# Kernel optimization log

Hardware: AMD Instinct MI355X
Metric: run time of the kernel (lower is better)

## Reference

```python
import jax, jax.numpy as jnp
import numpy as np
import math

DIM = 1024
NUM_HEADS = 16
HEAD_DIM = DIM // NUM_HEADS  # 64
LAYER_IDX = 12
LAMBDA_INIT = 0.8 - 0.6 * math.exp(-0.3 * (LAYER_IDX - 1))
LN_EPS = 1e-5


def setup_inputs() -> dict:
    key = jax.random.key(0)
    ks = jax.random.split(key, 11)
    B, S = 2, 2048
    x = jax.random.normal(ks[0], (B, S, DIM), dtype=jnp.float32)
    s = 1.0 / math.sqrt(DIM)
    Wq = jax.random.normal(ks[1], (DIM, 2 * DIM), dtype=jnp.float32) * s
    Wk = jax.random.normal(ks[2], (DIM, 2 * DIM), dtype=jnp.float32) * s
    Wv = jax.random.normal(ks[3], (DIM, DIM), dtype=jnp.float32) * s
    Wo = jax.random.normal(ks[4], (DIM, DIM), dtype=jnp.float32) * s
    lambda_q1 = jax.random.normal(ks[5], (HEAD_DIM,), dtype=jnp.float32) * 0.1
    lambda_k1 = jax.random.normal(ks[6], (HEAD_DIM,), dtype=jnp.float32) * 0.1
    lambda_q2 = jax.random.normal(ks[7], (HEAD_DIM,), dtype=jnp.float32) * 0.1
    lambda_k2 = jax.random.normal(ks[8], (HEAD_DIM,), dtype=jnp.float32) * 0.1
    gamma = jnp.ones((DIM,), dtype=jnp.float32)
    beta = jnp.zeros((DIM,), dtype=jnp.float32)
    return {"x": x, "Wq": Wq, "Wk": Wk, "Wv": Wv, "Wo": Wo,
            "lambda_q1": lambda_q1, "lambda_k1": lambda_k1,
            "lambda_q2": lambda_q2, "lambda_k2": lambda_k2,
            "gamma": gamma, "beta": beta}


def reference(x, Wq, Wk, Wv, Wo, lambda_q1, lambda_k1, lambda_q2, lambda_k2, gamma, beta):
    B, S, _ = x.shape
    scaling = HEAD_DIM ** (-0.5)
    # projections: [B,S,H,2d] / [B,S,H,d] -> [B,H,S,*]
    Q = (x @ Wq).reshape(B, S, NUM_HEADS, 2 * HEAD_DIM).transpose(0, 2, 1, 3)
    K = (x @ Wk).reshape(B, S, NUM_HEADS, 2 * HEAD_DIM).transpose(0, 2, 1, 3)
    V = (x @ Wv).reshape(B, S, NUM_HEADS, HEAD_DIM).transpose(0, 2, 1, 3)
    # lambda scalar
    lamb = (jnp.exp(jnp.sum(lambda_q1 * lambda_k1))
            - jnp.exp(jnp.sum(lambda_q2 * lambda_k2)) + LAMBDA_INIT)
    Q1, Q2 = jnp.split(Q, 2, axis=-1)
    K1, K2 = jnp.split(K, 2, axis=-1)
    A1 = jnp.einsum('bhqd,bhkd->bhqk', Q1, K1) * scaling
    A2 = jnp.einsum('bhqd,bhkd->bhqk', Q2, K2) * scaling
    attn = jax.nn.softmax(A1, axis=-1) - lamb * jax.nn.softmax(A2, axis=-1)
    out = jnp.einsum('bhqk,bhkd->bhqd', attn, V)  # [B,H,S,d]
    out = out.transpose(0, 2, 1, 3).reshape(B, S, DIM)
    out = out @ Wo
    # LayerNorm
    mu = jnp.mean(out, axis=-1, keepdims=True)
    var = jnp.var(out, axis=-1, keepdims=True)
    out = (out - mu) * jax.lax.rsqrt(var + LN_EPS) * gamma + beta
    return out
```

## Files before the change

### kernel.cpp

```cpp
#include <hip/hip_runtime.h>
#include <hip/hip_bf16.h>

typedef short bf16x8 __attribute__((ext_vector_type(8)));
typedef float f32x4 __attribute__((ext_vector_type(4)));
typedef unsigned short us4v __attribute__((ext_vector_type(4)));
typedef unsigned int uint2v __attribute__((ext_vector_type(2)));

#define DEV static __device__ __forceinline__

DEV float bf2f(unsigned short u){ unsigned int x = ((unsigned int)u)<<16; float f; __builtin_memcpy(&f,&x,4); return f; }
DEV unsigned short f2bf(float f){ unsigned int x; __builtin_memcpy(&x,&f,4); x = (x + 0x7fffu + ((x>>16)&1u)) >> 16; return (unsigned short)x; }

#if __has_builtin(__builtin_amdgcn_perm)
DEV unsigned int pack_trunc(float lo, float hi){
  unsigned int a, b;
  __builtin_memcpy(&a, &lo, 4);
  __builtin_memcpy(&b, &hi, 4);
  return __builtin_amdgcn_perm(b, a, 0x07060302u);
}
#else
DEV unsigned int pack_trunc(float lo, float hi){
  unsigned int a, b;
  __builtin_memcpy(&a, &lo, 4);
  __builtin_memcpy(&b, &hi, 4);
  return (b & 0xffff0000u) | (a >> 16);
}
#endif

DEV void stor(unsigned short* p, float v){ *p = f2bf(v); }
DEV void stor(float* p, float v){ *p = v; }

#if __has_builtin(__builtin_amdgcn_exp2f)
DEV float fexp2(float x){ return __builtin_amdgcn_exp2f(x); }
#else
DEV float fexp2(float x){ return exp2f(x); }
#endif

#if __has_builtin(__builtin_amdgcn_permlane32_swap)
DEV uint2v pl32(unsigned int a, unsigned int b){ return __builtin_amdgcn_permlane32_swap(a, b, false, false); }
#else
DEV uint2v pl32(unsigned int a, unsigned int b){
  unsigned int sa = (unsigned int)__shfl_xor((int)a, 32);
  unsigned int sb = (unsigned int)__shfl_xor((int)b, 32);
  bool hi = (threadIdx.x & 32) != 0;
  uint2v r; r[0] = hi ? sb : a; r[1] = hi ? b : sa; return r;
}
#endif
#if __has_builtin(__builtin_amdgcn_permlane16_swap)
DEV uint2v pl16(unsigned int a, unsigned int b){ return __builtin_amdgcn_permlane16_swap(a, b, false, false); }
#else
DEV uint2v pl16(unsigned int a, unsigned int b){
  unsigned int sa = (unsigned int)__shfl_xor((int)a, 16);
  unsigned int sb = (unsigned int)__shfl_xor((int)b, 16);
  bool hi = (threadIdx.x & 16) != 0;
  uint2v r; r[0] = hi ? sb : a; r[1] = hi ? b : sa; return r;
}
#endif

#define GLOAD_LDS16(gptr, lptr) \
  __builtin_amdgcn_global_load_lds((__attribute__((address_space(1))) void*)(gptr), \
      (__attribute__((address_space(3))) void*)(lptr), 16, 0, 0)

template<typename OutT>
__global__ __launch_bounds__(256) void gemm_bt(
    const unsigned short* __restrict__ A,
    const unsigned short* __restrict__ Bt,
    OutT* __restrict__ C, int M, int N, int K)
{
  __shared__ unsigned short As[128*32];
  __shared__ unsigned short Bs[128*32];
  const int tid = threadIdx.x;
  const int w = tid>>6, l = tid&63, g = l>>4, q = l&15;
  const int m0 = blockIdx.x*128, n0 = blockIdx.y*128;
  f32x4 acc[4][4];
  const f32x4 fz = {0.f,0.f,0.f,0.f};
  for (int i=0;i<4;i++) for(int j=0;j<4;j++) acc[i][j] = fz;
  for (int k0 = 0; k0 < K; k0 += 32) {
    __syncthreads();
    #pragma unroll
    for (int r = 0; r < 2; ++r) {
      int p = r*4096 + tid*16;
      int row = p>>6, colb = p&63;
      const char* ga = (const char*)(A  + (size_t)(m0+row)*K + k0) + colb;
      const char* gb = (const char*)(Bt + (size_t)(n0+row)*K + k0) + colb;
      GLOAD_LDS16(ga, (char*)As + r*4096 + w*1024);
      GLOAD_LDS16(gb, (char*)Bs + r*4096 + w*1024);
    }
    __syncthreads();
    bf16x8 af[4], bfr[4];
    #pragma unroll
    for (int i=0;i<4;i++){
      af[i]  = *(const bf16x8*)&As[((w>>1)*64 + i*16 + q)*32 + g*8];
      bfr[i] = *(const bf16x8*)&Bs[((w&1)*64 + i*16 + q)*32 + g*8];
    }
    #pragma unroll
    for (int i=0;i<4;i++)
      #pragma unroll
      for (int j=0;j<4;j++)
        acc[i][j] = __builtin_amdgcn_mfma_f32_16x16x32_bf16(af[i], bfr[j], acc[i][j], 0,0,0);
  }
  #pragma unroll
  for (int i=0;i<4;i++)
    #pragma unroll
    for (int j=0;j<4;j++)
      #pragma unroll
      for (int v=0;v<4;v++){
        int row = m0 + (w>>1)*64 + i*16 + g*4 + v;
        int col = n0 + (w&1)*64 + j*16 + q;
        stor(&C[(size_t)row*N + col], acc[i][j][v]);
      }
}

__global__ __launch_bounds__(256) void gemm_bt_64(
    const unsigned short* __restrict__ A,
    const unsigned short* __restrict__ Bt,
    float* __restrict__ C, int M, int N, int K)
{
  __shared__ unsigned short As[64*32];
  __shared__ unsigned short Bs[128*32];
  const int tid = threadIdx.x;
  const int w = tid>>6, l = tid&63, g = l>>4, q = l&15;
  const int m0 = blockIdx.x*64, n0 = blockIdx.y*128;
  f32x4 acc[4][2];
  const f32x4 fz = {0.f,0.f,0.f,0.f};
  for (int i=0;i<4;i++) for(int j=0;j<2;j++) acc[i][j] = fz;
  for (int k0 = 0; k0 < K; k0 += 32) {
    __syncthreads();
    {
      int row = tid>>2, colb = (tid&3)*16;
      const char* ga = (const char*)(A + (size_t)(m0+row)*K + k0) + colb;
      GLOAD_LDS16(ga, (char*)As + tid*16);
    }
    #pragma unroll
    for (int r = 0; r < 2; ++r) {
      int p = r*4096 + tid*16;
      int row = p>>6, colb = p&63;
      const char* gb = (const char*)(Bt + (size_t)(n0+row)*K + k0) + colb;
      GLOAD_LDS16(gb, (char*)Bs + r*4096 + w*1024);
    }
    __syncthreads();
    bf16x8 af[4], bfr[2];
    #pragma unroll
    for (int i=0;i<4;i++) af[i] = *(const bf16x8*)&As[(i*16 + q)*32 + g*8];
    #pragma unroll
    for (int j=0;j<2;j++) bfr[j] = *(const bf16x8*)&Bs[(w*32 + j*16 + q)*32 + g*8];
    #pragma unroll
    for (int i=0;i<4;i++)
      #pragma unroll
      for (int j=0;j<2;j++)
        acc[i][j] = __builtin_amdgcn_mfma_f32_16x16x32_bf16(af[i], bfr[j], acc[i][j], 0,0,0);
  }
  #pragma unroll
  for (int i=0;i<4;i++)
    #pragma unroll
    for (int j=0;j<2;j++)
      #pragma unroll
      for (int v=0;v<4;v++){
        int row = m0 + i*16 + g*4 + v;
        int col = n0 + w*32 + j*16 + q;
        C[(size_t)row*N + col] = acc[i][j][v];
      }
}

__global__ __launch_bounds__(256,4) void diff_attn(
    const unsigned short* __restrict__ Qp,
    const unsigned short* __restrict__ Kp,
    const unsigned short* __restrict__ Vt,
    unsigned short* __restrict__ ao1,
    unsigned short* __restrict__ ao2)
{
  const int LDQ = 5120;
  __shared__ unsigned short Ks0[64*64];
  __shared__ unsigned short Ks1[64*64];
  __shared__ unsigned short Vs0[64*64];
  __shared__ unsigned short Vs1[64*64];
  const int tid = threadIdx.x, w = tid>>6, l = tid&63, g = l>>4, q = l&15;
  const int qb = blockIdx.x, h = blockIdx.y;
  const int s = blockIdx.z >> 1, b = blockIdx.z & 1;
  const int b2048 = b*2048;
  const int qrow0 = b2048 + qb*128 + w*32;
  const f32x4 fz = {0.f,0.f,0.f,0.f};
  const short one_bf = (short)0x3f80;
  const bf16x8 ones = {one_bf,one_bf,one_bf,one_bf,one_bf,one_bf,one_bf,one_bf};
  unsigned short* aout = s ? ao2 : ao1;

  bf16x8 qf[2][2];
  #pragma unroll
  for (int qh=0; qh<2; ++qh){
    const unsigned short* qp = Qp + (size_t)(qrow0 + qh*16 + q)*LDQ + h*128 + s*64;
    #pragma unroll
    for (int kf=0;kf<2;kf++)
      qf[qh][kf] = *(const bf16x8*)(qp + kf*32 + g*8);
  }
  f32x4 acc[2][4];
  f32x4 acc_s[2];
  #pragma unroll
  for (int qh=0;qh<2;qh++){
    acc_s[qh]=fz;
    #pragma unroll
    for (int i=0;i<4;i++) acc[qh][i]=fz;
  }

  auto STAGE = [&](unsigned short* Kd, unsigned short* Vd, int kt){
    #pragma unroll
    for (int ii=0; ii<2; ++ii){
      int krow = w*16 + ii*8 + (l>>3);
      int gr = (l&7) ^ (krow&7);
      const unsigned short* src = Kp + (size_t)(b2048 + kt + krow)*LDQ + h*128 + s*64 + gr*8;
      GLOAD_LDS16(src, (char*)Kd + (w*16 + ii*8)*128);
    }
    #pragma unroll
    for (int jj=0; jj<2; ++jj){
      int vrow = w*16 + jj*8 + (l>>3);
      int gr = (l&7) ^ (vrow&7);
      const unsigned short* src = Vt + (size_t)(h*64 + vrow)*4096 + b2048 + kt + gr*8;
      GLOAD_LDS16(src, (char*)Vd + (w*16 + jj*8)*128);
    }
  };

  auto COMPUTE = [&](const unsigned short* Kr, const unsigned short* Vr){
    const int sw = q & 7;
    unsigned int cc[2][4][2];
    #pragma unroll
    for (int fn=0; fn<4; ++fn) {
      const unsigned short* kr = Kr + (fn*16 + q)*64;
      bf16x8 kb0 = *(const bf16x8*)&kr[((0+g)^sw)*8];
      bf16x8 kb1 = *(const bf16x8*)&kr[((4+g)^sw)*8];
      f32x4 z[2];
      __builtin_amdgcn_s_setprio(1);
      #pragma unroll
      for (int qh=0; qh<2; ++qh){
        f32x4 a = fz;
        a = __builtin_amdgcn_mfma_f32_16x16x32_bf16(kb0, qf[qh][0], a, 0,0,0);
        a = __builtin_amdgcn_mfma_f32_16x16x32_bf16(kb1, qf[qh][1], a, 0,0,0);
        z[qh] = a;
      }
      __builtin_amdgcn_s_setprio(0);
      #pragma unroll
      for (int qh=0; qh<2; ++qh){
        cc[qh][fn][0] = pack_trunc(fexp2(z[qh][0]), fexp2(z[qh][1]));
        cc[qh][fn][1] = pack_trunc(fexp2(z[qh][2]), fexp2(z[qh][3]));
      }
    }

    bf16x8 pa[2][2];
    #pragma unroll
    for (int qh=0; qh<2; ++qh)
      #pragma unroll
      for (int kh=0; kh<2; ++kh){
        unsigned int* u = (unsigned int*)&pa[qh][kh];
        #pragma unroll
        for (int j=0;j<2;j++){
          uint2v d = pl32(cc[qh][2*kh][j], cc[qh][2*kh+1][j]);
          uint2v e = pl16(d[0], d[1]);
          u[j] = e[0]; u[2+j] = e[1];
        }
      }

    __builtin_amdgcn_s_setprio(1);
    #pragma unroll
    for (int kh=0; kh<2; ++kh){
      #pragma unroll
      for (int qh=0; qh<2; ++qh)
        acc_s[qh] = __builtin_amdgcn_mfma_f32_16x16x32_bf16(pa[qh][kh], ones, acc_s[qh], 0,0,0);
      #pragma unroll
      for (int fd=0; fd<4; ++fd){
        bf16x8 vb = *(const bf16x8*)&Vr[(fd*16+q)*64 + ((kh*4+g)^sw)*8];
        #pragma unroll
        for (int qh=0; qh<2; ++qh)
          acc[qh][fd] = __builtin_amdgcn_mfma_f32_16x16x32_bf16(pa[qh][kh], vb, acc[qh][fd], 0,0,0);
      }
    }
    __builtin_amdgcn_s_setprio(0);
  };

  STAGE(Ks0, Vs0, 0);
  __syncthreads();

  for (int t=0; t<32; t+=2) {
    STAGE(Ks1, Vs1, (t+1)*64);
    COMPUTE(Ks0, Vs0);
    __syncthreads();
    if (t+2 < 32) STAGE(Ks0, Vs0, (t+2)*64);
    COMPUTE(Ks1, Vs1);
    if (t+2 < 32) __syncthreads();
  }

  #pragma unroll
  for (int qh=0; qh<2; ++qh){
    float inv[4];
    #pragma unroll
    for (int i=0;i<4;i++) inv[i] = 1.0f/acc_s[qh][i];
    #pragma unroll
    for (int fd=0; fd<4; ++fd)
      #pragma unroll
      for (int i=0;i<4;i++){
        int row = qrow0 + qh*16 + g*4 + i;
        int col = h*64 + fd*16 + q;
        aout[(size_t)row*1024 + col] = f2bf(acc[qh][fd][i]*inv[i]);
      }
  }
}

__global__ __launch_bounds__(256) void combine_k(
    const unsigned short* __restrict__ a1, const unsigned short* __restrict__ a2,
    const float* __restrict__ lambp, unsigned short* __restrict__ out, int n)
{
  int i = (blockIdx.x*256 + threadIdx.x)*8;
  if (i >= n) return;
  float lamb = lambp[0];
  bf16x8 v1 = *(const bf16x8*)(a1+i), v2 = *(const bf16x8*)(a2+i);
  bf16x8 o;
  #pragma unroll
  for (int e=0;e<8;e++)
    o[e] = (short)f2bf(bf2f((unsigned short)v1[e]) - lamb*bf2f((unsigned short)v2[e]));
  *(bf16x8*)(out+i) = o;
}

__global__ __launch_bounds__(256) void f32_to_bf16_k(const float* __restrict__ in, unsigned short* __restrict__ out, int n){
  int i = (blockIdx.x*256 + threadIdx.x)*4;
  if (i >= n) return;
  float4 vv = *(const float4*)(in + i);
  us4v o; o[0]=f2bf(vv.x); o[1]=f2bf(vv.y); o[2]=f2bf(vv.z); o[3]=f2bf(vv.w);
  *(us4v*)(out + i) = o;
}

__global__ void transpose_weights(const float* __restrict__ Wq, const float* __restrict__ Wk,
                                  const float* __restrict__ Wv, const float* __restrict__ Wo,
                                  unsigned short* __restrict__ WcatT, unsigned short* __restrict__ WoT,
                                  float qscale){
  __shared__ unsigned short t[32][33];
  int bid = blockIdx.x;
  const float* in; unsigned short* out; int C; float scale = 1.0f;
  if (bid < 2048){ in = Wq; out = WcatT;             C = 2048; scale = qscale; }
  else if (bid < 4096){ in = Wk; out = WcatT + 2048*1024; C = 2048; bid -= 2048; }
  else if (bid < 5120){ in = Wv; out = WcatT + 4096*1024; C = 1024; bid -= 4096; }
  else { in = Wo; out = WoT; C = 1024; bid -= 5120; }
  int xt = (C == 2048) ? (bid & 63) : (bid & 31);
  int yt = (C == 2048) ? (bid >> 6) : (bid >> 5);
  int c0 = xt*32, r0 = yt*32;
  int x = threadIdx.x, y = threadIdx.y;
  #pragma unroll
  for (int d=0; d<32; d+=8) t[y+d][x] = f2bf(in[(size_t)(r0+y+d)*C + c0 + x] * scale);
  __syncthreads();
  #pragma unroll
  for (int d=0; d<32; d+=8) out[(size_t)(c0+y+d)*1024 + r0 + x] = t[x][y+d];
}

__global__ void transpose_bf16_ld(const unsigned short* __restrict__ in, unsigned short* __restrict__ out, int R, int C, int ldin){
  __shared__ unsigned short t[32][33];
  int c0 = blockIdx.x*32, r0 = blockIdx.y*32;
  int x = threadIdx.x, y = threadIdx.y;
  #pragma unroll
  for (int d=0; d<32; d+=8) t[y+d][x] = in[(size_t)(r0+y+d)*ldin + c0 + x];
  __syncthreads();
  #pragma unroll
  for (int d=0; d<32; d+=8) out[(size_t)(c0+y+d)*R + r0 + x] = t[x][y+d];
}

__global__ void lamb_k(const float* lq1, const float* lk1, const float* lq2, const float* lk2, float* out){
  int i = threadIdx.x;
  float a = lq1[i]*lk1[i], c = lq2[i]*lk2[i];
  #pragma unroll
  for (int o=32;o>0;o>>=1){ a += __shfl_down(a,o); c += __shfl_down(c,o); }
  if (i==0) out[0] = expf(a) - expf(c) + 0.7778700995592560f;
}

__global__ __launch_bounds__(256) void ln_k(const float* __restrict__ in, const float* __restrict__ gam,
                                            const float* __restrict__ bet, float* __restrict__ out){
  int row = blockIdx.x, t = threadIdx.x;
  const float4* rp = (const float4*)(in + (size_t)row*1024);
  float4 v4 = rp[t];
  float s = v4.x+v4.y+v4.z+v4.w;
  float ss = v4.x*v4.x+v4.y*v4.y+v4.z*v4.z+v4.w*v4.w;
  #pragma unroll
  for (int o=1;o<64;o<<=1){ s += __shfl_xor(s,o); ss += __shfl_xor(ss,o); }
  __shared__ float red[8];
  int w = t>>6, l = t&63;
  if (l==0){ red[w]=s; red[4+w]=ss; }
  __syncthreads();
  s = red[0]+red[1]+red[2]+red[3];
  ss = red[4]+red[5]+red[6]+red[7];
  float mean = s*(1.0f/1024.0f);
  float var = ss*(1.0f/1024.0f) - mean*mean;
  float rstd = rsqrtf(var + 1e-5f);
  float4 gv = ((const float4*)gam)[t], bv = ((const float4*)bet)[t];
  float4 o;
  o.x = (v4.x-mean)*rstd*gv.x + bv.x;
  o.y = (v4.y-mean)*rstd*gv.y + bv.y;
  o.z = (v4.z-mean)*rstd*gv.z + bv.z;
  o.w = (v4.w-mean)*rstd*gv.w + bv.w;
  ((float4*)(out + (size_t)row*1024))[t] = o;
}

extern "C" void kernel_launch(void* const* d_in, const int* in_sizes, int n_in,
                              void* d_out, int out_size, void* d_ws, size_t ws_size,
                              hipStream_t stream) {
  const float* x     = (const float*)d_in[0];
  const float* Wq    = (const float*)d_in[1];
  const float* Wk    = (const float*)d_in[2];
  const float* Wv    = (const float*)d_in[3];
  const float* Wo    = (const float*)d_in[4];
  const float* lq1   = (const float*)d_in[5];
  const float* lk1   = (const float*)d_in[6];
  const float* lq2   = (const float*)d_in[7];
  const float* lk2   = (const float*)d_in[8];
  const float* gamma = (const float*)d_in[9];
  const float* beta  = (const float*)d_in[10];
  float* out = (float*)d_out;

  char* ws = (char*)d_ws;
  unsigned short* xb    = (unsigned short*)(ws);
  unsigned short* WcatT = (unsigned short*)(ws + 8388608);
  unsigned short* WoT   = (unsigned short*)(ws + 18874368);
  unsigned short* QKV   = (unsigned short*)(ws + 20971520);
  unsigned short* Vtb   = (unsigned short*)(ws + 62914560);
  unsigned short* AO1   = (unsigned short*)(ws + 71303168);
  unsigned short* AO2   = (unsigned short*)(ws + 79691776);
  unsigned short* AOc   = (unsigned short*)(ws + 88080384);
  float*          proj  = (float*)(ws + 20971520);
  float*          lambp = (float*)(ws + 96468992);

  const float QSCALE = 0.125f * 1.4426950408889634f;
  dim3 tb(32,8);
  f32_to_bf16_k<<<4096, 256, 0, stream>>>(x, xb, 4194304);
  transpose_weights<<<6144, tb, 0, stream>>>(Wq, Wk, Wv, Wo, WcatT, WoT, QSCALE);
  lamb_k<<<1, 64, 0, stream>>>(lq1, lk1, lq2, lk2, lambp);

  gemm_bt<unsigned short><<<dim3(32,40), 256, 0, stream>>>(xb, WcatT, QKV, 4096, 5120, 1024);
  transpose_bf16_ld<<<dim3(32,128), tb, 0, stream>>>(QKV + 4096, Vtb, 4096, 1024, 5120);

  diff_attn<<<dim3(16,16,4), 256, 0, stream>>>(QKV, QKV + 2048, Vtb, AO1, AO2);
  combine_k<<<2048, 256, 0, stream>>>(AO1, AO2, lambp, AOc, 4194304);

  gemm_bt_64<<<dim3(64,8), 256, 0, stream>>>(AOc, WoT, proj, 4096, 1024, 1024);
  ln_k<<<4096, 256, 0, stream>>>(proj, gamma, beta, out);
}
```

Baseline: 197.6 us.

## Fold lambda combine into attention epilogue and Wo GEMM load; merge prep kernels

Result: no change. 194.5 us (-1.6%).

```diff
diff --git a/kernel.cpp b/kernel.cpp
--- a/kernel.cpp
+++ b/kernel.cpp
@@ -111,8 +111,9 @@
       }
 }
 
-__global__ __launch_bounds__(256) void gemm_bt_64(
-    const unsigned short* __restrict__ A,
+__global__ __launch_bounds__(256) void gemm_wo_fused(
+    const unsigned short* __restrict__ A1,
+    const unsigned short* __restrict__ A2,
     const unsigned short* __restrict__ Bt,
     float* __restrict__ C, int M, int N, int K)
 {
@@ -127,9 +128,16 @@
   for (int k0 = 0; k0 < K; k0 += 32) {
     __syncthreads();
     {
-      int row = tid>>2, colb = (tid&3)*16;
-      const char* ga = (const char*)(A + (size_t)(m0+row)*K + k0) + colb;
-      GLOAD_LDS16(ga, (char*)As + tid*16);
+      int row = tid>>2, c8 = (tid&3)*8;
+      const unsigned short* p1 = A1 + (size_t)(m0+row)*K + k0 + c8;
+      const unsigned short* p2 = A2 + (size_t)(m0+row)*K + k0 + c8;
+      bf16x8 v1 = *(const bf16x8*)p1;
+      bf16x8 v2 = *(const bf16x8*)p2;
+      bf16x8 o;
+      #pragma unroll
+      for (int e=0;e<8;e++)
+        o[e] = (short)f2bf(bf2f((unsigned short)v1[e]) + bf2f((unsigned short)v2[e]));
+      *(bf16x8*)&As[row*32 + c8] = o;
     }
     #pragma unroll
     for (int r = 0; r < 2; ++r) {
@@ -166,6 +174,7 @@
     const unsigned short* __restrict__ Qp,
     const unsigned short* __restrict__ Kp,
     const unsigned short* __restrict__ Vt,
+    const float* __restrict__ lambp,
     unsigned short* __restrict__ ao1,
     unsigned short* __restrict__ ao2)
 {
@@ -286,11 +295,12 @@
     if (t+2 < 32) __syncthreads();
   }
 
+  float sgn = s ? -lambp[0] : 1.0f;
   #pragma unroll
   for (int qh=0; qh<2; ++qh){
     float inv[4];
     #pragma unroll
-    for (int i=0;i<4;i++) inv[i] = 1.0f/acc_s[qh][i];
+    for (int i=0;i<4;i++) inv[i] = sgn/acc_s[qh][i];
     #pragma unroll
     for (int fd=0; fd<4; ++fd)
       #pragma unroll
@@ -302,49 +312,51 @@
   }
 }
 
-__global__ __launch_bounds__(256) void combine_k(
-    const unsigned short* __restrict__ a1, const unsigned short* __restrict__ a2,
-    const float* __restrict__ lambp, unsigned short* __restrict__ out, int n)
+__global__ __launch_bounds__(256) void prep_k(
+    const float* __restrict__ x, unsigned short* __restrict__ xb,
+    const float* __restrict__ Wq, const float* __restrict__ Wk,
+    const float* __restrict__ Wv, const float* __restrict__ Wo,
+    unsigned short* __restrict__ WcatT, unsigned short* __restrict__ WoT,
+    float qscale,
+    const float* __restrict__ lq1, const float* __restrict__ lk1,
+    const float* __restrict__ lq2, const float* __restrict__ lk2,
+    float* __restrict__ lambp)
 {
-  int i = (blockIdx.x*256 + threadIdx.x)*8;
-  if (i >= n) return;
-  float lamb = lambp[0];
-  bf16x8 v1 = *(const bf16x8*)(a1+i), v2 = *(const bf16x8*)(a2+i);
-  bf16x8 o;
-  #pragma unroll
-  for (int e=0;e<8;e++)
-    o[e] = (short)f2bf(bf2f((unsigned short)v1[e]) - lamb*bf2f((unsigned short)v2[e]));
-  *(bf16x8*)(out+i) = o;
-}
-
-__global__ __launch_bounds__(256) void f32_to_bf16_k(const float* __restrict__ in, unsigned short* __restrict__ out, int n){
-  int i = (blockIdx.x*256 + threadIdx.x)*4;
-  if (i >= n) return;
-  float4 vv = *(const float4*)(in + i);
-  us4v o; o[0]=f2bf(vv.x); o[1]=f2bf(vv.y); o[2]=f2bf(vv.z); o[3]=f2bf(vv.w);
-  *(us4v*)(out + i) = o;
-}
-
-__global__ void transpose_weights(const float* __restrict__ Wq, const float* __restrict__ Wk,
-                                  const float* __restrict__ Wv, const float* __restrict__ Wo,
-                                  unsigned short* __restrict__ WcatT, unsigned short* __restrict__ WoT,
-                                  float qscale){
-  __shared__ unsigned short t[32][33];
   int bid = blockIdx.x;
-  const float* in; unsigned short* out; int C; float scale = 1.0f;
-  if (bid < 2048){ in = Wq; out = WcatT;             C = 2048; scale = qscale; }
-  else if (bid < 4096){ in = Wk; out = WcatT + 2048*1024; C = 2048; bid -= 2048; }
-  else if (bid < 5120){ in = Wv; out = WcatT + 4096*1024; C = 1024; bid -= 4096; }
-  else { in = Wo; out = WoT; C = 1024; bid -= 5120; }
-  int xt = (C == 2048) ? (bid & 63) : (bid & 31);
-  int yt = (C == 2048) ? (bid >> 6) : (bid >> 5);
-  int c0 = xt*32, r0 = yt*32;
-  int x = threadIdx.x, y = threadIdx.y;
-  #pragma unroll
-  for (int d=0; d<32; d+=8) t[y+d][x] = f2bf(in[(size_t)(r0+y+d)*C + c0 + x] * scale);
-  __syncthreads();
-  #pragma unroll
-  for (int d=0; d<32; d+=8) out[(size_t)(c0+y+d)*1024 + r0 + x] = t[x][y+d];
+  int tid = threadIdx.x;
+  if (bid < 4096){
+    int i = (bid*256 + tid)*4;
+    float4 vv = *(const float4*)(x + i);
+    us4v o; o[0]=f2bf(vv.x); o[1]=f2bf(vv.y); o[2]=f2bf(vv.z); o[3]=f2bf(vv.w);
+    *(us4v*)(xb + i) = o;
+    return;
+  }
+  if (bid < 10240){
+    __shared__ unsigned short t[32][33];
+    int wb = bid - 4096;
+    const float* in; unsigned short* out; int C; float scale = 1.0f;
+    if (wb < 2048){ in = Wq; out = WcatT;             C = 2048; scale = qscale; }
+    else if (wb < 4096){ in = Wk; out = WcatT + 2048*1024; C = 2048; wb -= 2048; }
+    else if (wb < 5120){ in = Wv; out = WcatT + 4096*1024; C = 1024; wb -= 4096; }
+    else { in = Wo; out = WoT; C = 1024; wb -= 5120; }
+    int xt = (C == 2048) ? (wb & 63) : (wb & 31);
+    int yt = (C == 2048) ? (wb >> 6) : (wb >> 5);
+    int c0 = xt*32, r0 = yt*32;
+    int xx = tid & 31, yy = tid >> 5;
+    #pragma unroll
+    for (int d=0; d<32; d+=8) t[yy+d][xx] = f2bf(in[(size_t)(r0+yy+d)*C + c0 + xx] * scale);
+    __syncthreads();
+    #pragma unroll
+    for (int d=0; d<32; d+=8) out[(size_t)(c0+yy+d)*1024 + r0 + xx] = t[xx][yy+d];
+    return;
+  }
+  {
+    int i = tid & 63;
+    float a = lq1[i]*lk1[i], c = lq2[i]*lk2[i];
+    #pragma unroll
+    for (int o=32;o>0;o>>=1){ a += __shfl_down(a,o); c += __shfl_down(c,o); }
+    if (tid==0) lambp[0] = expf(a) - expf(c) + 0.7778700995592560f;
+  }
 }
 
 __global__ void transpose_bf16_ld(const unsigned short* __restrict__ in, unsigned short* __restrict__ out, int R, int C, int ldin){
@@ -356,14 +368,6 @@
   __syncthreads();
   #pragma unroll
   for (int d=0; d<32; d+=8) out[(size_t)(c0+y+d)*R + r0 + x] = t[x][y+d];
-}
-
-__global__ void lamb_k(const float* lq1, const float* lk1, const float* lq2, const float* lk2, float* out){
-  int i = threadIdx.x;
-  float a = lq1[i]*lk1[i], c = lq2[i]*lk2[i];
-  #pragma unroll
-  for (int o=32;o>0;o>>=1){ a += __shfl_down(a,o); c += __shfl_down(c,o); }
-  if (i==0) out[0] = expf(a) - expf(c) + 0.7778700995592560f;
 }
 
 __global__ __launch_bounds__(256) void ln_k(const float* __restrict__ in, const float* __restrict__ gam,
@@ -417,22 +421,19 @@
   unsigned short* Vtb   = (unsigned short*)(ws + 62914560);
   unsigned short* AO1   = (unsigned short*)(ws + 71303168);
   unsigned short* AO2   = (unsigned short*)(ws + 79691776);
-  unsigned short* AOc   = (unsigned short*)(ws + 88080384);
   float*          proj  = (float*)(ws + 20971520);
   float*          lambp = (float*)(ws + 96468992);
 
   const float QSCALE = 0.125f * 1.4426950408889634f;
   dim3 tb(32,8);
-  f32_to_bf16_k<<<4096, 256, 0, stream>>>(x, xb, 4194304);
-  transpose_weights<<<6144, tb, 0, stream>>>(Wq, Wk, Wv, Wo, WcatT, WoT, QSCALE);
-  lamb_k<<<1, 64, 0, stream>>>(lq1, lk1, lq2, lk2, lambp);
+  prep_k<<<10241, 256, 0, stream>>>(x, xb, Wq, Wk, Wv, Wo, WcatT, WoT, QSCALE,
+                                    lq1, lk1, lq2, lk2, lambp);
 
   gemm_bt<unsigned short><<<dim3(32,40), 256, 0, stream>>>(xb, WcatT, QKV, 4096, 5120, 1024);
   transpose_bf16_ld<<<dim3(32,128), tb, 0, stream>>>(QKV + 4096, Vtb, 4096, 1024, 5120);
 
-  diff_attn<<<dim3(16,16,4), 256, 0, stream>>>(QKV, QKV + 2048, Vtb, AO1, AO2);
-  combine_k<<<2048, 256, 0, stream>>>(AO1, AO2, lambp, AOc, 4194304);
-
-  gemm_bt_64<<<dim3(64,8), 256, 0, stream>>>(AOc, WoT, proj, 4096, 1024, 1024);
+  diff_attn<<<dim3(16,16,4), 256, 0, stream>>>(QKV, QKV + 2048, Vtb, lambp, AO1, AO2);
+
+  gemm_wo_fused<<<dim3(64,8), 256, 0, stream>>>(AO1, AO2, WoT, proj, 4096, 1024, 1024);
   ln_k<<<4096, 256, 0, stream>>>(proj, gamma, beta, out);
 }
```
